# Kernel optimization log

Measured on AMD Instinct MI355X. Metric: run time of the kernel, lower is better.

Reference implementation:

```python
import jax, jax.numpy as jnp
import numpy as np

B, T, D, H, L = 64, 256, 1024, 1024, 4

def setup_inputs() -> dict:
    key = jax.random.key(0)
    k1, k2, k3 = jax.random.split(key, 3)
    x = jax.random.normal(k1, (B, T, D), dtype=jnp.float32)
    # Keras LSTMCell params per layer: kernel [D,4H], recurrent_kernel [H,4H], bias [4H]
    Ws = jax.random.normal(k2, (L, D, 4 * H), dtype=jnp.float32) * (1.0 / np.sqrt(D))
    Us = jax.random.normal(k3, (L, H, 4 * H), dtype=jnp.float32) * (1.0 / np.sqrt(H))
    # unit_forget_bias=True: forget-gate bias initialized to 1
    b = np.zeros((L, 4 * H), dtype=np.float32)
    b[:, H:2 * H] = 1.0
    return {"x": x, "Ws": Ws, "Us": Us, "bs": jnp.asarray(b)}

def _lstm_layer(x, W, U, b):
    # Precompute input projection for all timesteps: [B,T,4H]
    xz = jnp.einsum('btd,dg->btg', x, W) + b
    h0 = jnp.zeros((x.shape[0], U.shape[0]), x.dtype)
    c0 = jnp.zeros_like(h0)
    def step(carry, zt):
        h, c = carry
        z = zt + h @ U  # [B,4H]
        i, f, g, o = jnp.split(z, 4, axis=-1)
        i = jax.nn.sigmoid(i)
        f = jax.nn.sigmoid(f)
        g = jnp.tanh(g)
        o = jax.nn.sigmoid(o)
        c_new = f * c + i * g
        h_new = o * jnp.tanh(c_new)
        return (h_new, c_new), h_new
    _, hs = jax.lax.scan(step, (h0, c0), jnp.swapaxes(xz, 0, 1))  # hs: [T,B,H]
    return jnp.swapaxes(hs, 0, 1)  # [B,T,H]

def reference(x, Ws, Us, bs):
    seq = x
    for l in range(Ws.shape[0]):  # small fixed layer loop
        seq = _lstm_layer(seq, Ws[l], Us[l], bs[l])
    return seq
```

## Files before the change

kernel.cpp:

```cpp
#include <hip/hip_runtime.h>
#include <stdint.h>
#include <stddef.h>

typedef _Float16 f16;
typedef _Float16 f16x8 __attribute__((ext_vector_type(8)));
typedef float f32x4 __attribute__((ext_vector_type(4)));
typedef int i32x4 __attribute__((ext_vector_type(4)));

#define MFMA16(a, b, c) __builtin_amdgcn_mfma_f32_16x16x32_f16((a), (b), (c), 0, 0, 0)

static constexpr int kB = 64;
static constexpr int kT = 256;
static constexpr int kD = 1024;
static constexpr int kH = 1024;
static constexpr int kG = 4096;
static constexpr int kSlot = 64 * 1024;
static constexpr int kNSlots = kT + 1;
static constexpr size_t kHistE = (size_t)kNSlots * kSlot;

__device__ __forceinline__ float fast_sigmoid(float x) {
  return __builtin_amdgcn_rcpf(1.f + __expf(-x));
}
__device__ __forceinline__ float fast_tanh(float x) {
  x = fminf(9.f, fmaxf(-9.f, x));
  const float e = __expf(2.f * x);
  return (e - 1.f) * __builtin_amdgcn_rcpf(e + 1.f);
}

__global__ void x_perm_cvt(const float* __restrict__ x, f16* __restrict__ xp) {
  const size_t id = (size_t)blockIdx.x * 256 + threadIdx.x;
  const int d8 = (int)(id & 127) << 3;
  const int b = (int)(id >> 7) & 63;
  const int t = (int)(id >> 13);
  const float* s = x + (((size_t)b * kT + t) << 10) + d8;
  float4 a = *(const float4*)(s);
  float4 c = *(const float4*)(s + 4);
  f16x8 o;
  o[0] = (f16)a.x; o[1] = (f16)a.y; o[2] = (f16)a.z; o[3] = (f16)a.w;
  o[4] = (f16)c.x; o[5] = (f16)c.y; o[6] = (f16)c.z; o[7] = (f16)c.w;
  *(f16x8*)(xp + (size_t)t * kSlot + (size_t)(d8 >> 3) * 512 + b * 8) = o;
}

__global__ void transpose_cvt_z(const float* __restrict__ src, f16* __restrict__ dst) {
  __shared__ float tile[32][33];
  const int z = blockIdx.z;
  const int c0 = blockIdx.x * 32;
  const int r0 = blockIdx.y * 32;
  const float* s = src + (size_t)z * kD * kG;
  f16* d = dst + (size_t)z * kG * kD;
  for (int rr = threadIdx.y; rr < 32; rr += 8)
    tile[rr][threadIdx.x] = s[(size_t)(r0 + rr) * kG + c0 + threadIdx.x];
  __syncthreads();
  for (int cc = threadIdx.y; cc < 32; cc += 8)
    d[(size_t)(c0 + cc) * kD + r0 + threadIdx.x] = (f16)tile[threadIdx.x][cc];
}

__launch_bounds__(1024, 1)
__global__ void lstm_scan2(const f16* __restrict__ below_lo,
                           const f16* __restrict__ Wt_lo, const f16* __restrict__ Ut_lo,
                           const f16* __restrict__ Wt_hi, const f16* __restrict__ Ut_hi,
                           f16* __restrict__ hist_lo, f16* __restrict__ hist_hi,
                           int* __restrict__ flags_lo, int* __restrict__ flags_hi,
                           const float* __restrict__ bias_lo,
                           const float* __restrict__ bias_hi,
                           float* __restrict__ out32) {
  __shared__ f16 Cw[8192 * 8];
  __shared__ f16 red0h[2][12 * 64 * 4];
  __shared__ f16 red1h[2][12 * 64 * 4];
  __shared__ f16 hstage[4][16][8];
  __shared__ int lds_ready[2];

  const int bid = blockIdx.x;
  const int layerbit = bid & 1;
  const int wgl = bid >> 1;
  const int hbase = wgl * 8;
  const int tid = threadIdx.x;
  const int l = tid & 63, w = tid >> 6;
  const int lr = l & 15, lq = l >> 4;
  const int bw = w & 3, kw = w >> 2;

  const f16* Wt = layerbit ? Wt_hi : Wt_lo;
  const f16* Ut = layerbit ? Ut_hi : Ut_lo;
  f16* own_hist = layerbit ? hist_hi : hist_lo;
  const f16* below_base = layerbit ? (hist_lo + kSlot) : below_lo;
  const int* fpoll_own = layerbit ? flags_hi : flags_lo;
  const int* fpoll_below = flags_lo;
  int* fpub = (layerbit ? flags_hi : flags_lo) + (wgl * 4 + bw);
  const float* bias = layerbit ? bias_hi : bias_lo;

  if (tid == 0) {
    lds_ready[0] = layerbit ? -1 : (1 << 30);
    lds_ready[1] = 0;
  }

#pragma unroll
  for (int ff = 0; ff < 8; ++ff) {
    const int f = tid * 8 + ff;
    const int x = f >> 12, kkg = (f >> 6) & 63, fl = f & 63;
    const int flr = fl & 15, flq = fl >> 4;
    const int r = x * 16 + flr;
    const int grow = (r >> 3) * 1024 + hbase + (r & 7);
    const f16* src = (kkg < 32) ? Wt : Ut;
    *(f16x8*)&Cw[f * 8] =
        *(const f16x8*)(src + (size_t)grow * 1024 + (kkg & 31) * 32 + flq * 8);
  }

  float bv0 = 0.f, bv1 = 0.f;
  if (kw == 0) {
    bv0 = bias[((lr < 8) ? 0 : 1024) + hbase + (lr & 7)];
    bv1 = bias[((lr < 8) ? 2048 : 3072) + hbase + (lr & 7)];
  }
  __syncthreads();

  const int brow = bw * 16 + lq * 4;
  const int ugl = hbase + (lr & 7);
  const int* pollp = ((w == 0) ? fpoll_below : fpoll_own) + l * 8;
  const int row = bw * 16 + lr;

  float c_reg[4] = {0.f, 0.f, 0.f, 0.f};

#pragma unroll 1
  for (int t = 0; t < kT; ++t) {
    if (w == 0) {
      if (layerbit) {
        const int tgt = t + 1;
        for (;;) {
          i32x4 pa, pb;
          asm volatile("global_load_dwordx4 %0, %2, off sc0 sc1\n\t"
                       "global_load_dwordx4 %1, %3, off sc0 sc1\n\t"
                       "s_waitcnt vmcnt(0)"
                       : "=v"(pa), "=v"(pb) : "v"(pollp), "v"(pollp + 4) : "memory");
          const bool ok = pa[0] >= tgt && pa[1] >= tgt && pa[2] >= tgt && pa[3] >= tgt &&
                          pb[0] >= tgt && pb[1] >= tgt && pb[2] >= tgt && pb[3] >= tgt;
          if (__all(ok)) break;
        }
        __asm__ __volatile__("" ::: "memory");
        *(volatile int*)&lds_ready[0] = t;
      }
    } else if (w == 8) {
      const int tgt = t;
      for (;;) {
        i32x4 pa, pb;
        asm volatile("global_load_dwordx4 %0, %2, off sc0 sc1\n\t"
                     "global_load_dwordx4 %1, %3, off sc0 sc1\n\t"
                     "s_waitcnt vmcnt(0)"
                     : "=v"(pa), "=v"(pb) : "v"(pollp), "v"(pollp + 4) : "memory");
        const bool ok = pa[0] >= tgt && pa[1] >= tgt && pa[2] >= tgt && pa[3] >= tgt &&
                        pb[0] >= tgt && pb[1] >= tgt && pb[2] >= tgt && pb[3] >= tgt;
        if (__all(ok)) break;
      }
      __asm__ __volatile__("" ::: "memory");
      *(volatile int*)&lds_ready[1] = t;
    }
    {
      volatile int* rdy = &lds_ready[kw >> 1];
      while (*rdy < t) __builtin_amdgcn_s_sleep(1);
      __asm__ __volatile__("" ::: "memory");
    }

    const f16* hsrc = (kw < 2) ? (below_base + (size_t)t * kSlot)
                               : (own_hist + (size_t)t * kSlot);
    const f16* hp = hsrc + (size_t)((kw & 1) * 64 + lq) * 512 + row * 8;
    f16x8 ha[16];
#pragma unroll
    for (int ii = 0; ii < 16; ++ii)
      ha[ii] = *(const f16x8*)(hp + (size_t)ii * 2048);

    f32x4 acc0 = {}, acc1 = {};
    const int kkb = kw * 16;
#pragma unroll
    for (int ii = 0; ii < 16; ++ii) {
      const f16x8 b0 = *(const f16x8*)&Cw[((kkb + ii) * 64 + l) * 8];
      const f16x8 b1 = *(const f16x8*)&Cw[((4096 + (kkb + ii) * 64) + l) * 8];
      acc0 = MFMA16(ha[ii], b0, acc0);
      acc1 = MFMA16(ha[ii], b1, acc1);
    }

    if (kw != 0) {
      const int rb = ((w - 4) * 64 + l) * 4;
#pragma unroll
      for (int j = 0; j < 4; ++j) {
        red0h[t & 1][rb + j] = (f16)acc0[j];
        red1h[t & 1][rb + j] = (f16)acc1[j];
      }
    }
    __syncthreads();

    if (kw == 0) {
      f32x4 s0 = acc0, s1 = acc1;
#pragma unroll
      for (int q = 0; q < 3; ++q) {
        const int rb = ((q * 4 + bw) * 64 + l) * 4;
#pragma unroll
        for (int j = 0; j < 4; ++j) {
          s0[j] += (float)red0h[t & 1][rb + j];
          s1[j] += (float)red1h[t & 1][rb + j];
        }
      }

      float hv[4];
#pragma unroll
      for (int j = 0; j < 4; ++j) {
        const float z0 = s0[j] + bv0;
        const float z1 = s1[j] + bv1;
        const float q0 = __shfl_xor(z0, 8);
        const float q1 = __shfl_xor(z1, 8);
        const float zi = (lr & 8) ? q0 : z0;
        const float zf = (lr & 8) ? z0 : q0;
        const float zg = (lr & 8) ? q1 : z1;
        const float zo = (lr & 8) ? z1 : q1;
        const float iv = fast_sigmoid(zi);
        const float fv = fast_sigmoid(zf);
        const float gv = fast_tanh(zg);
        const float ov = fast_sigmoid(zo);
        const float cn = fv * c_reg[j] + iv * gv;
        c_reg[j] = cn;
        hv[j] = ov * fast_tanh(cn);
      }

      if (lr < 8) {
#pragma unroll
        for (int j = 0; j < 4; ++j)
          hstage[w][lq * 4 + j][lr] = (f16)hv[j];
      }
      if (l < 16) {
        const f16x8 hrow = *(const f16x8*)&hstage[w][l][0];
        f16* dst = own_hist + (size_t)(t + 1) * kSlot +
                   ((size_t)wgl * 64 + bw * 16 + l) * 8;
        asm volatile("global_store_dwordx4 %0, %1, off sc0 sc1"
                     :: "v"(dst), "v"(hrow) : "memory");
      }
      asm volatile("s_waitcnt vmcnt(0)" ::: "memory");
      if (l == 0) {
        const int val = t + 1;
        asm volatile("global_store_dword %0, %1, off sc0 sc1"
                     :: "v"(fpub), "v"(val) : "memory");
      }
      if (out32 && layerbit && lr < 8) {
#pragma unroll
        for (int j = 0; j < 4; ++j)
          out32[((size_t)(brow + j) * kT + t) * kH + ugl] = hv[j];
      }
    }
  }
}

extern "C" void kernel_launch(void* const* d_in, const int* in_sizes, int n_in,
                              void* d_out, int out_size, void* d_ws, size_t ws_size,
                              hipStream_t stream) {
  (void)in_sizes; (void)n_in; (void)out_size; (void)ws_size;
  const float* x = (const float*)d_in[0];
  const float* Ws = (const float*)d_in[1];
  const float* Us = (const float*)d_in[2];
  const float* bs = (const float*)d_in[3];
  char* ws = (char*)d_ws;

  const size_t kLayerW = (size_t)kG * kD * 2;
  const size_t kHistB = kHistE * 2;
  const size_t WT_OFF = 0;
  const size_t UT_OFF = WT_OFF + 4 * kLayerW;
  const size_t XP_OFF = UT_OFF + 4 * kLayerW;
  const size_t HH_OFF = XP_OFF + (size_t)kT * kSlot * 2;
  const size_t FL_OFF = HH_OFF + 4 * kHistB;

  f16* Wt = (f16*)(ws + WT_OFF);
  f16* Ut = (f16*)(ws + UT_OFF);
  f16* xp = (f16*)(ws + XP_OFF);
  int* fl = (int*)(ws + FL_OFF);

  f16* hist[4];
  for (int i = 0; i < 4; ++i) hist[i] = (f16*)(ws + HH_OFF + i * kHistB);

  x_perm_cvt<<<8192, 256, 0, stream>>>(x, xp);
  transpose_cvt_z<<<dim3(kG / 32, kD / 32, 4), dim3(32, 8), 0, stream>>>(Ws, Wt);
  transpose_cvt_z<<<dim3(kG / 32, kD / 32, 4), dim3(32, 8), 0, stream>>>(Us, Ut);
  for (int i = 0; i < 4; ++i)
    hipMemsetAsync(ws + HH_OFF + i * kHistB, 0, (size_t)kSlot * 2, stream);
  hipMemsetAsync(ws + FL_OFF, 0, 4 * 512 * 4, stream);

  lstm_scan2<<<256, 1024, 0, stream>>>(
      xp, Wt, Ut, Wt + (size_t)kG * kD, Ut + (size_t)kG * kD,
      hist[0], hist[1], fl, fl + 512,
      bs, bs + kG, (float*)nullptr);
  lstm_scan2<<<256, 1024, 0, stream>>>(
      hist[1] + kSlot, Wt + 2 * (size_t)kG * kD, Ut + 2 * (size_t)kG * kD,
      Wt + 3 * (size_t)kG * kD, Ut + 3 * (size_t)kG * kD,
      hist[2], hist[3], fl + 1024, fl + 1536,
      bs + 2 * kG, bs + 3 * kG, (float*)d_out);
}
```

Before: 3.701 ms.

## Shrink scan blocks to four waves, drop LDS K-reduction, per-batch-slice flag polling

The persistent LSTM scan kernel goes from 16 waves per block with a 4-way K split and LDS reduction to 4 waves, each owning a 16-row batch slice and running the full K loop itself. The cross-block flag protocol becomes per-batch-slice flags: each wave polls only the 128 producers for its own slice, and the independent input-projection term is computed before waiting on the recurrent dependency (or the reverse for the upper layer). This removes the per-step __syncthreads, the fp16 LDS reduction and the LDS-ready handshake, so waves progress independently. In exchange each wave does four times the serial MFMA and load work per step, with much less in flight per CU.

```diff
diff --git a/kernel.cpp b/kernel.cpp
--- a/kernel.cpp
+++ b/kernel.cpp
@@ -5,7 +5,6 @@
 typedef _Float16 f16;
 typedef _Float16 f16x8 __attribute__((ext_vector_type(8)));
 typedef float f32x4 __attribute__((ext_vector_type(4)));
-typedef int i32x4 __attribute__((ext_vector_type(4)));
 
 #define MFMA16(a, b, c) __builtin_amdgcn_mfma_f32_16x16x32_f16((a), (b), (c), 0, 0, 0)
 
@@ -55,47 +54,64 @@
     d[(size_t)(c0 + cc) * kD + r0 + threadIdx.x] = (f16)tile[threadIdx.x][cc];
 }
 
-__launch_bounds__(1024, 1)
+#define POLLF(PP, TGT)                                                        \
+  for (;;) {                                                                  \
+    unsigned long long fv;                                                    \
+    asm volatile("global_load_dwordx2 %0, %1, off sc0 sc1\n\t"                \
+                 "s_waitcnt vmcnt(0)"                                         \
+                 : "=v"(fv) : "v"(PP) : "memory");                            \
+    if (__all((int)(fv & 0xffffffffu) >= (TGT) && (int)(fv >> 32) >= (TGT)))  \
+      break;                                                                  \
+  }
+
+#define TERM_LOOP(hp, kkg0, A0, A1)                                           \
+  _Pragma("unroll 1")                                                         \
+  for (int base = 0; base < 32; base += 8) {                                  \
+    f16x8 ha[8];                                                              \
+    _Pragma("unroll")                                                         \
+    for (int j = 0; j < 8; ++j)                                               \
+      ha[j] = *(const f16x8*)((hp) + (size_t)(base + j) * 2048);              \
+    _Pragma("unroll")                                                         \
+    for (int j = 0; j < 8; ++j) {                                             \
+      const int kkg = (kkg0) + base + j;                                      \
+      const f16x8 w0 = *(const f16x8*)&Cw[(kkg * 64 + l) * 8];                \
+      const f16x8 w1 = *(const f16x8*)&Cw[((4096 + kkg * 64) + l) * 8];       \
+      (A0) = MFMA16(ha[j], w0, (A0));                                         \
+      (A1) = MFMA16(ha[j], w1, (A1));                                         \
+    }                                                                         \
+  }
+
+__launch_bounds__(256, 1)
 __global__ void lstm_scan2(const f16* __restrict__ below_lo,
                            const f16* __restrict__ Wt_lo, const f16* __restrict__ Ut_lo,
                            const f16* __restrict__ Wt_hi, const f16* __restrict__ Ut_hi,
                            f16* __restrict__ hist_lo, f16* __restrict__ hist_hi,
-                           int* __restrict__ flags_lo, int* __restrict__ flags_hi,
+                           int* __restrict__ flags_lo,
+                           int* __restrict__ flags_hi,
                            const float* __restrict__ bias_lo,
                            const float* __restrict__ bias_hi,
                            float* __restrict__ out32) {
   __shared__ f16 Cw[8192 * 8];
-  __shared__ f16 red0h[2][12 * 64 * 4];
-  __shared__ f16 red1h[2][12 * 64 * 4];
   __shared__ f16 hstage[4][16][8];
-  __shared__ int lds_ready[2];
 
   const int bid = blockIdx.x;
   const int layerbit = bid & 1;
   const int wgl = bid >> 1;
   const int hbase = wgl * 8;
   const int tid = threadIdx.x;
-  const int l = tid & 63, w = tid >> 6;
+  const int l = tid & 63, bw = tid >> 6;
   const int lr = l & 15, lq = l >> 4;
-  const int bw = w & 3, kw = w >> 2;
 
   const f16* Wt = layerbit ? Wt_hi : Wt_lo;
   const f16* Ut = layerbit ? Ut_hi : Ut_lo;
   f16* own_hist = layerbit ? hist_hi : hist_lo;
   const f16* below_base = layerbit ? (hist_lo + kSlot) : below_lo;
-  const int* fpoll_own = layerbit ? flags_hi : flags_lo;
-  const int* fpoll_below = flags_lo;
-  int* fpub = (layerbit ? flags_hi : flags_lo) + (wgl * 4 + bw);
+  int* flags_own = layerbit ? flags_hi : flags_lo;
   const float* bias = layerbit ? bias_hi : bias_lo;
 
-  if (tid == 0) {
-    lds_ready[0] = layerbit ? -1 : (1 << 30);
-    lds_ready[1] = 0;
-  }
-
-#pragma unroll
-  for (int ff = 0; ff < 8; ++ff) {
-    const int f = tid * 8 + ff;
+#pragma unroll 1
+  for (int ff = 0; ff < 32; ++ff) {
+    const int f = ff * 256 + tid;
     const int x = f >> 12, kkg = (f >> 6) & 63, fl = f & 63;
     const int flr = fl & 15, flq = fl >> 4;
     const int r = x * 16 + flr;
@@ -104,143 +120,80 @@
     *(f16x8*)&Cw[f * 8] =
         *(const f16x8*)(src + (size_t)grow * 1024 + (kkg & 31) * 32 + flq * 8);
   }
-
-  float bv0 = 0.f, bv1 = 0.f;
-  if (kw == 0) {
-    bv0 = bias[((lr < 8) ? 0 : 1024) + hbase + (lr & 7)];
-    bv1 = bias[((lr < 8) ? 2048 : 3072) + hbase + (lr & 7)];
-  }
+  const float bv0 = bias[((lr < 8) ? 0 : 1024) + hbase + (lr & 7)];
+  const float bv1 = bias[((lr < 8) ? 2048 : 3072) + hbase + (lr & 7)];
   __syncthreads();
 
+  const int row8 = (bw * 16 + lr) * 8;
   const int brow = bw * 16 + lq * 4;
   const int ugl = hbase + (lr & 7);
-  const int* pollp = ((w == 0) ? fpoll_below : fpoll_own) + l * 8;
-  const int row = bw * 16 + lr;
+  int* fpub = flags_own + bw * 128 + wgl;
+  const int* pollo = flags_own + bw * 128 + 2 * l;
+  const int* pollb = flags_lo + bw * 128 + 2 * l;
 
   float c_reg[4] = {0.f, 0.f, 0.f, 0.f};
 
 #pragma unroll 1
   for (int t = 0; t < kT; ++t) {
-    if (w == 0) {
-      if (layerbit) {
-        const int tgt = t + 1;
-        for (;;) {
-          i32x4 pa, pb;
-          asm volatile("global_load_dwordx4 %0, %2, off sc0 sc1\n\t"
-                       "global_load_dwordx4 %1, %3, off sc0 sc1\n\t"
-                       "s_waitcnt vmcnt(0)"
-                       : "=v"(pa), "=v"(pb) : "v"(pollp), "v"(pollp + 4) : "memory");
-          const bool ok = pa[0] >= tgt && pa[1] >= tgt && pa[2] >= tgt && pa[3] >= tgt &&
-                          pb[0] >= tgt && pb[1] >= tgt && pb[2] >= tgt && pb[3] >= tgt;
-          if (__all(ok)) break;
-        }
-        __asm__ __volatile__("" ::: "memory");
-        *(volatile int*)&lds_ready[0] = t;
-      }
-    } else if (w == 8) {
-      const int tgt = t;
-      for (;;) {
-        i32x4 pa, pb;
-        asm volatile("global_load_dwordx4 %0, %2, off sc0 sc1\n\t"
-                     "global_load_dwordx4 %1, %3, off sc0 sc1\n\t"
-                     "s_waitcnt vmcnt(0)"
-                     : "=v"(pa), "=v"(pb) : "v"(pollp), "v"(pollp + 4) : "memory");
-        const bool ok = pa[0] >= tgt && pa[1] >= tgt && pa[2] >= tgt && pa[3] >= tgt &&
-                        pb[0] >= tgt && pb[1] >= tgt && pb[2] >= tgt && pb[3] >= tgt;
-        if (__all(ok)) break;
-      }
-      __asm__ __volatile__("" ::: "memory");
-      *(volatile int*)&lds_ready[1] = t;
-    }
-    {
-      volatile int* rdy = &lds_ready[kw >> 1];
-      while (*rdy < t) __builtin_amdgcn_s_sleep(1);
-      __asm__ __volatile__("" ::: "memory");
-    }
-
-    const f16* hsrc = (kw < 2) ? (below_base + (size_t)t * kSlot)
-                               : (own_hist + (size_t)t * kSlot);
-    const f16* hp = hsrc + (size_t)((kw & 1) * 64 + lq) * 512 + row * 8;
-    f16x8 ha[16];
+    f32x4 a0 = {}, a1 = {}, b0 = {}, b1 = {};
+
+    if (!layerbit) {
+      const f16* hb = below_base + (size_t)t * kSlot + lq * 512 + row8;
+      TERM_LOOP(hb, 0, b0, b1)
+      POLLF(pollo, t)
+      const f16* ho = own_hist + (size_t)t * kSlot + lq * 512 + row8;
+      TERM_LOOP(ho, 32, a0, a1)
+    } else {
+      POLLF(pollo, t)
+      const f16* ho = own_hist + (size_t)t * kSlot + lq * 512 + row8;
+      TERM_LOOP(ho, 32, a0, a1)
+      POLLF(pollb, t + 1)
+      const f16* hb = below_base + (size_t)t * kSlot + lq * 512 + row8;
+      TERM_LOOP(hb, 0, b0, b1)
+    }
+
+    float hv[4];
 #pragma unroll
-    for (int ii = 0; ii < 16; ++ii)
-      ha[ii] = *(const f16x8*)(hp + (size_t)ii * 2048);
-
-    f32x4 acc0 = {}, acc1 = {};
-    const int kkb = kw * 16;
+    for (int j = 0; j < 4; ++j) {
+      const float z0 = a0[j] + b0[j] + bv0;
+      const float z1 = a1[j] + b1[j] + bv1;
+      const float q0 = __shfl_xor(z0, 8);
+      const float q1 = __shfl_xor(z1, 8);
+      const float zi = (lr & 8) ? q0 : z0;
+      const float zf = (lr & 8) ? z0 : q0;
+      const float zg = (lr & 8) ? q1 : z1;
+      const float zo = (lr & 8) ? z1 : q1;
+      const float iv = fast_sigmoid(zi);
+      const float fv = fast_sigmoid(zf);
+      const float gv = fast_tanh(zg);
+      const float ov = fast_sigmoid(zo);
+      const float cn = fv * c_reg[j] + iv * gv;
+      c_reg[j] = cn;
+      hv[j] = ov * fast_tanh(cn);
+    }
+
+    if (lr < 8) {
 #pragma unroll
-    for (int ii = 0; ii < 16; ++ii) {
-      const f16x8 b0 = *(const f16x8*)&Cw[((kkb + ii) * 64 + l) * 8];
-      const f16x8 b1 = *(const f16x8*)&Cw[((4096 + (kkb + ii) * 64) + l) * 8];
-      acc0 = MFMA16(ha[ii], b0, acc0);
-      acc1 = MFMA16(ha[ii], b1, acc1);
-    }
-
-    if (kw != 0) {
-      const int rb = ((w - 4) * 64 + l) * 4;
+      for (int j = 0; j < 4; ++j)
+        hstage[bw][lq * 4 + j][lr] = (f16)hv[j];
+    }
+    if (l < 16) {
+      const f16x8 hrow = *(const f16x8*)&hstage[bw][l][0];
+      f16* dst = own_hist + (size_t)(t + 1) * kSlot +
+                 ((size_t)wgl * 64 + bw * 16 + l) * 8;
+      asm volatile("global_store_dwordx4 %0, %1, off sc0 sc1"
+                   :: "v"(dst), "v"(hrow) : "memory");
+    }
+    asm volatile("s_waitcnt vmcnt(0)" ::: "memory");
+    if (l == 0) {
+      const int val = t + 1;
+      asm volatile("global_store_dword %0, %1, off sc0 sc1"
+                   :: "v"(fpub), "v"(val) : "memory");
+    }
+    if (out32 && layerbit && lr < 8) {
 #pragma unroll
-      for (int j = 0; j < 4; ++j) {
-        red0h[t & 1][rb + j] = (f16)acc0[j];
-        red1h[t & 1][rb + j] = (f16)acc1[j];
-      }
-    }
-    __syncthreads();
-
-    if (kw == 0) {
-      f32x4 s0 = acc0, s1 = acc1;
-#pragma unroll
-      for (int q = 0; q < 3; ++q) {
-        const int rb = ((q * 4 + bw) * 64 + l) * 4;
-#pragma unroll
-        for (int j = 0; j < 4; ++j) {
-          s0[j] += (float)red0h[t & 1][rb + j];
-          s1[j] += (float)red1h[t & 1][rb + j];
-        }
-      }
-
-      float hv[4];
-#pragma unroll
-      for (int j = 0; j < 4; ++j) {
-        const float z0 = s0[j] + bv0;
-        const float z1 = s1[j] + bv1;
-        const float q0 = __shfl_xor(z0, 8);
-        const float q1 = __shfl_xor(z1, 8);
-        const float zi = (lr & 8) ? q0 : z0;
-        const float zf = (lr & 8) ? z0 : q0;
-        const float zg = (lr & 8) ? q1 : z1;
-        const float zo = (lr & 8) ? z1 : q1;
-        const float iv = fast_sigmoid(zi);
-        const float fv = fast_sigmoid(zf);
-        const float gv = fast_tanh(zg);
-        const float ov = fast_sigmoid(zo);
-        const float cn = fv * c_reg[j] + iv * gv;
-        c_reg[j] = cn;
-        hv[j] = ov * fast_tanh(cn);
-      }
-
-      if (lr < 8) {
-#pragma unroll
-        for (int j = 0; j < 4; ++j)
-          hstage[w][lq * 4 + j][lr] = (f16)hv[j];
-      }
-      if (l < 16) {
-        const f16x8 hrow = *(const f16x8*)&hstage[w][l][0];
-        f16* dst = own_hist + (size_t)(t + 1) * kSlot +
-                   ((size_t)wgl * 64 + bw * 16 + l) * 8;
-        asm volatile("global_store_dwordx4 %0, %1, off sc0 sc1"
-                     :: "v"(dst), "v"(hrow) : "memory");
-      }
-      asm volatile("s_waitcnt vmcnt(0)" ::: "memory");
-      if (l == 0) {
-        const int val = t + 1;
-        asm volatile("global_store_dword %0, %1, off sc0 sc1"
-                     :: "v"(fpub), "v"(val) : "memory");
-      }
-      if (out32 && layerbit && lr < 8) {
-#pragma unroll
-        for (int j = 0; j < 4; ++j)
-          out32[((size_t)(brow + j) * kT + t) * kH + ugl] = hv[j];
-      }
+      for (int j = 0; j < 4; ++j)
+        out32[((size_t)(brow + j) * kT + t) * kH + ugl] = hv[j];
     }
   }
 }
@@ -278,11 +231,11 @@
     hipMemsetAsync(ws + HH_OFF + i * kHistB, 0, (size_t)kSlot * 2, stream);
   hipMemsetAsync(ws + FL_OFF, 0, 4 * 512 * 4, stream);
 
-  lstm_scan2<<<256, 1024, 0, stream>>>(
+  lstm_scan2<<<256, 256, 0, stream>>>(
       xp, Wt, Ut, Wt + (size_t)kG * kD, Ut + (size_t)kG * kD,
       hist[0], hist[1], fl, fl + 512,
       bs, bs + kG, (float*)nullptr);
-  lstm_scan2<<<256, 1024, 0, stream>>>(
+  lstm_scan2<<<256, 256, 0, stream>>>(
       hist[1] + kSlot, Wt + 2 * (size_t)kG * kD, Ut + 2 * (size_t)kG * kD,
       Wt + 3 * (size_t)kG * kD, Ut + 3 * (size_t)kG * kD,
       hist[2], hist[3], fl + 1024, fl + 1536,
```

Measured after the change: 8.657 ms. 2.34x slower.

## Replace flag-based step sync with sentinel-filled history polling

Applied to the files above, without the earlier changes.

Drops the per-wave flag publish/poll protocol and LDS ready counters. Instead, the history buffers are pre-filled with a 0x7F7F sentinel, and consumer waves spin on coherent loads of the h data itself until no sentinel remains. This removes the flag store, its vmcnt wait after each h store, and the intra-block LDS handoff from the recurrent critical path. In exchange it adds a large memset of all history slots, heavier polling traffic (16 vector loads per retry), and relies on stores of 16-byte rows being seen atomically and on 0x7F7F never occurring as a real fp16 h value.

```diff
diff --git a/kernel.cpp b/kernel.cpp
--- a/kernel.cpp
+++ b/kernel.cpp
@@ -5,7 +5,6 @@
 typedef _Float16 f16;
 typedef _Float16 f16x8 __attribute__((ext_vector_type(8)));
 typedef float f32x4 __attribute__((ext_vector_type(4)));
-typedef int i32x4 __attribute__((ext_vector_type(4)));
 
 #define MFMA16(a, b, c) __builtin_amdgcn_mfma_f32_16x16x32_f16((a), (b), (c), 0, 0, 0)
 
@@ -60,7 +59,6 @@
                            const f16* __restrict__ Wt_lo, const f16* __restrict__ Ut_lo,
                            const f16* __restrict__ Wt_hi, const f16* __restrict__ Ut_hi,
                            f16* __restrict__ hist_lo, f16* __restrict__ hist_hi,
-                           int* __restrict__ flags_lo, int* __restrict__ flags_hi,
                            const float* __restrict__ bias_lo,
                            const float* __restrict__ bias_hi,
                            float* __restrict__ out32) {
@@ -68,7 +66,6 @@
   __shared__ f16 red0h[2][12 * 64 * 4];
   __shared__ f16 red1h[2][12 * 64 * 4];
   __shared__ f16 hstage[4][16][8];
-  __shared__ int lds_ready[2];
 
   const int bid = blockIdx.x;
   const int layerbit = bid & 1;
@@ -83,15 +80,7 @@
   const f16* Ut = layerbit ? Ut_hi : Ut_lo;
   f16* own_hist = layerbit ? hist_hi : hist_lo;
   const f16* below_base = layerbit ? (hist_lo + kSlot) : below_lo;
-  const int* fpoll_own = layerbit ? flags_hi : flags_lo;
-  const int* fpoll_below = flags_lo;
-  int* fpub = (layerbit ? flags_hi : flags_lo) + (wgl * 4 + bw);
   const float* bias = layerbit ? bias_hi : bias_lo;
-
-  if (tid == 0) {
-    lds_ready[0] = layerbit ? -1 : (1 << 30);
-    lds_ready[1] = 0;
-  }
 
 #pragma unroll
   for (int ff = 0; ff < 8; ++ff) {
@@ -114,57 +103,43 @@
 
   const int brow = bw * 16 + lq * 4;
   const int ugl = hbase + (lr & 7);
-  const int* pollp = ((w == 0) ? fpoll_below : fpoll_own) + l * 8;
   const int row = bw * 16 + lr;
+  const bool needs_poll = layerbit || (kw >= 2);
 
   float c_reg[4] = {0.f, 0.f, 0.f, 0.f};
 
 #pragma unroll 1
   for (int t = 0; t < kT; ++t) {
-    if (w == 0) {
-      if (layerbit) {
-        const int tgt = t + 1;
-        for (;;) {
-          i32x4 pa, pb;
-          asm volatile("global_load_dwordx4 %0, %2, off sc0 sc1\n\t"
-                       "global_load_dwordx4 %1, %3, off sc0 sc1\n\t"
-                       "s_waitcnt vmcnt(0)"
-                       : "=v"(pa), "=v"(pb) : "v"(pollp), "v"(pollp + 4) : "memory");
-          const bool ok = pa[0] >= tgt && pa[1] >= tgt && pa[2] >= tgt && pa[3] >= tgt &&
-                          pb[0] >= tgt && pb[1] >= tgt && pb[2] >= tgt && pb[3] >= tgt;
-          if (__all(ok)) break;
-        }
-        __asm__ __volatile__("" ::: "memory");
-        *(volatile int*)&lds_ready[0] = t;
-      }
-    } else if (w == 8) {
-      const int tgt = t;
-      for (;;) {
-        i32x4 pa, pb;
-        asm volatile("global_load_dwordx4 %0, %2, off sc0 sc1\n\t"
-                     "global_load_dwordx4 %1, %3, off sc0 sc1\n\t"
-                     "s_waitcnt vmcnt(0)"
-                     : "=v"(pa), "=v"(pb) : "v"(pollp), "v"(pollp + 4) : "memory");
-        const bool ok = pa[0] >= tgt && pa[1] >= tgt && pa[2] >= tgt && pa[3] >= tgt &&
-                        pb[0] >= tgt && pb[1] >= tgt && pb[2] >= tgt && pb[3] >= tgt;
-        if (__all(ok)) break;
-      }
-      __asm__ __volatile__("" ::: "memory");
-      *(volatile int*)&lds_ready[1] = t;
-    }
-    {
-      volatile int* rdy = &lds_ready[kw >> 1];
-      while (*rdy < t) __builtin_amdgcn_s_sleep(1);
-      __asm__ __volatile__("" ::: "memory");
-    }
-
     const f16* hsrc = (kw < 2) ? (below_base + (size_t)t * kSlot)
                                : (own_hist + (size_t)t * kSlot);
     const f16* hp = hsrc + (size_t)((kw & 1) * 64 + lq) * 512 + row * 8;
+
     f16x8 ha[16];
-#pragma unroll
-    for (int ii = 0; ii < 16; ++ii)
-      ha[ii] = *(const f16x8*)(hp + (size_t)ii * 2048);
+    if (needs_poll) {
+      for (;;) {
+#pragma unroll
+        for (int ii = 0; ii < 16; ++ii)
+          asm volatile("global_load_dwordx4 %0, %1, off sc0 sc1"
+                       : "=v"(ha[ii]) : "v"(hp + (size_t)ii * 2048) : "memory");
+        asm volatile("s_waitcnt vmcnt(0)" ::: "memory");
+        __builtin_amdgcn_sched_barrier(0);
+        bool ok = true;
+#pragma unroll
+        for (int ii = 0; ii < 16; ++ii) {
+#pragma unroll
+          for (int e = 0; e < 8; e += 2) {
+            const f16 ev = ha[ii][e];
+            const unsigned short bb = __builtin_bit_cast(unsigned short, ev);
+            ok = ok && (bb != 0x7F7F);
+          }
+        }
+        if (__all(ok)) break;
+      }
+    } else {
+#pragma unroll
+      for (int ii = 0; ii < 16; ++ii)
+        ha[ii] = *(const f16x8*)(hp + (size_t)ii * 2048);
+    }
 
     f32x4 acc0 = {}, acc1 = {};
     const int kkb = kw * 16;
@@ -230,12 +205,6 @@
         asm volatile("global_store_dwordx4 %0, %1, off sc0 sc1"
                      :: "v"(dst), "v"(hrow) : "memory");
       }
-      asm volatile("s_waitcnt vmcnt(0)" ::: "memory");
-      if (l == 0) {
-        const int val = t + 1;
-        asm volatile("global_store_dword %0, %1, off sc0 sc1"
-                     :: "v"(fpub), "v"(val) : "memory");
-      }
       if (out32 && layerbit && lr < 8) {
 #pragma unroll
         for (int j = 0; j < 4; ++j)
@@ -261,12 +230,10 @@
   const size_t UT_OFF = WT_OFF + 4 * kLayerW;
   const size_t XP_OFF = UT_OFF + 4 * kLayerW;
   const size_t HH_OFF = XP_OFF + (size_t)kT * kSlot * 2;
-  const size_t FL_OFF = HH_OFF + 4 * kHistB;
 
   f16* Wt = (f16*)(ws + WT_OFF);
   f16* Ut = (f16*)(ws + UT_OFF);
   f16* xp = (f16*)(ws + XP_OFF);
-  int* fl = (int*)(ws + FL_OFF);
 
   f16* hist[4];
   for (int i = 0; i < 4; ++i) hist[i] = (f16*)(ws + HH_OFF + i * kHistB);
@@ -274,17 +241,19 @@
   x_perm_cvt<<<8192, 256, 0, stream>>>(x, xp);
   transpose_cvt_z<<<dim3(kG / 32, kD / 32, 4), dim3(32, 8), 0, stream>>>(Ws, Wt);
   transpose_cvt_z<<<dim3(kG / 32, kD / 32, 4), dim3(32, 8), 0, stream>>>(Us, Ut);
-  for (int i = 0; i < 4; ++i)
+  for (int i = 0; i < 4; ++i) {
     hipMemsetAsync(ws + HH_OFF + i * kHistB, 0, (size_t)kSlot * 2, stream);
-  hipMemsetAsync(ws + FL_OFF, 0, 4 * 512 * 4, stream);
+    hipMemsetAsync(ws + HH_OFF + i * kHistB + (size_t)kSlot * 2, 0x7F,
+                   (size_t)kT * kSlot * 2, stream);
+  }
 
   lstm_scan2<<<256, 1024, 0, stream>>>(
       xp, Wt, Ut, Wt + (size_t)kG * kD, Ut + (size_t)kG * kD,
-      hist[0], hist[1], fl, fl + 512,
+      hist[0], hist[1],
       bs, bs + kG, (float*)nullptr);
   lstm_scan2<<<256, 1024, 0, stream>>>(
       hist[1] + kSlot, Wt + 2 * (size_t)kG * kD, Ut + 2 * (size_t)kG * kD,
       Wt + 3 * (size_t)kG * kD, Ut + 3 * (size_t)kG * kD,
-      hist[2], hist[3], fl + 1024, fl + 1536,
+      hist[2], hist[3],
       bs + 2 * kG, bs + 3 * kG, (float*)d_out);
 }
```

New measurement: 3.249 ms, median of 2. -12.2%, faster.
